# Kernel tuning notes

Measured on AMD Instinct MI355X. Metric: run time of the kernel, lower is better.

The kernel has to match this reference:

```python
import jax, jax.numpy as jnp
import numpy as np
import math

SENTINEL = 1.0e6  # eta/phi value assigned to inactive (pt<=0) objects
BIG = 1.0e6       # dR placeholder for non-lower-triangular entries


def _remove_duplicates(objs, threshold):
    """objs: (B, n, 3) with columns (pt, eta, phi). Zeros out objects that
    are within dR < threshold of a later object in the group (faithful to
    the TF strictly-lower-triangular / reduce over rows logic)."""
    n = objs.shape[1]
    active = objs[..., 0] > 0.0                              # (B, n)
    eta = jnp.where(active, objs[..., 1], SENTINEL)
    phi = jnp.where(active, objs[..., 2], SENTINEL)
    deta = eta[:, :, None] - eta[:, None, :]                 # (B, n, n)
    dphi = jnp.mod(phi[:, :, None] - phi[:, None, :] + math.pi,
                   2.0 * math.pi) - math.pi
    dr2 = deta * deta + dphi * dphi
    # strictly lower triangular mask (row i > col j), same as
    # logical_not(band_part(ones, 0, -1)) in TF
    tri = jnp.tril(jnp.ones((n, n), dtype=bool), k=-1)       # (n, n)
    # safe sqrt: only evaluate where the mask keeps the value
    dr = jnp.sqrt(jnp.where(tri, dr2, 1.0))
    replaced = jnp.where(tri, dr, BIG)                       # (B, n, n)
    # TF reduce_any(..., axis=0) per event -> axis=1 of batched tensor
    duplicates = jnp.any(replaced < threshold, axis=1)       # (B, n)
    return jnp.where(duplicates[..., None], 0.0, objs)


def duplicate_removal(x, threshold):
    jets = _remove_duplicates(x[:, 0:6], threshold)
    electrons = _remove_duplicates(x[:, 6:9], threshold)
    muons = _remove_duplicates(x[:, 9:12], threshold)
    photons = _remove_duplicates(x[:, 12:15], threshold)
    met = x[:, 15:16]
    return jnp.concatenate([jets, electrons, muons, photons, met], axis=1)


def setup_inputs() -> dict:
    key = jax.random.key(0)
    x = jax.random.normal(key, (1000000, 16, 3), dtype=jnp.float32)
    return {"x": x}


def reference(x):
    return duplicate_removal(x, 0.05)
```

## Files before the change

kernel.cpp:

```cpp
#include <hip/hip_runtime.h>
#include <math.h>

#define PI_F    3.14159274101257324e0f
#define TWOPI_F 6.28318548202514648e0f
#define SENT_F  1000000.0f

template <int OFF, int N>
__device__ __forceinline__ unsigned group_dup(const float* __restrict__ r) {
    float e[N], p[N];
#pragma unroll
    for (int k = 0; k < N; ++k) {
        float pt = r[3 * (OFF + k) + 0];
        bool act = pt > 0.0f;
        e[k] = act ? r[3 * (OFF + k) + 1] : SENT_F;
        p[k] = act ? r[3 * (OFF + k) + 2] : SENT_F;
    }
    unsigned dup = 0;
#pragma unroll
    for (int j = 0; j < N - 1; ++j) {
        bool d = false;
#pragma unroll
        for (int i = j + 1; i < N; ++i) {
            float deta = e[i] - e[j];
            float dd   = (p[i] - p[j]) + PI_F;
            float m    = fmodf(dd, TWOPI_F);
            m = (m < 0.0f) ? (m + TWOPI_F) : m;
            float dphi = m - PI_F;
            float dr2 = __fadd_rn(__fmul_rn(deta, deta), __fmul_rn(dphi, dphi));
            float dr  = __fsqrt_rn(dr2);
            d = d || (dr < 0.05f);
        }
        if (d) dup |= (1u << (OFF + j));
    }
    return dup;
}

__global__ __launch_bounds__(256) void dup_removal_kernel(
    const float4* __restrict__ in, float4* __restrict__ out, int B) {
    int row = blockIdx.x * blockDim.x + threadIdx.x;
    if (row >= B) return;

    const float4* src = in + (size_t)row * 12;
    float4* dst = out + (size_t)row * 12;

    float r[48];
#pragma unroll
    for (int k = 0; k < 12; ++k) {
        float4 v = src[k];
        r[4 * k + 0] = v.x;
        r[4 * k + 1] = v.y;
        r[4 * k + 2] = v.z;
        r[4 * k + 3] = v.w;
    }

    unsigned dup = 0;
    dup |= group_dup<0, 6>(r);
    dup |= group_dup<6, 3>(r);
    dup |= group_dup<9, 3>(r);
    dup |= group_dup<12, 3>(r);

#pragma unroll
    for (int o = 0; o < 15; ++o) {
        bool z = (dup >> o) & 1u;
        r[3 * o + 0] = z ? 0.0f : r[3 * o + 0];
        r[3 * o + 1] = z ? 0.0f : r[3 * o + 1];
        r[3 * o + 2] = z ? 0.0f : r[3 * o + 2];
    }

#pragma unroll
    for (int k = 0; k < 12; ++k) {
        float4 v;
        v.x = r[4 * k + 0];
        v.y = r[4 * k + 1];
        v.z = r[4 * k + 2];
        v.w = r[4 * k + 3];
        dst[k] = v;
    }
}

extern "C" void kernel_launch(void* const* d_in, const int* in_sizes, int n_in,
                              void* d_out, int out_size, void* d_ws, size_t ws_size,
                              hipStream_t stream) {
    const float4* x = (const float4*)d_in[0];
    float4* out = (float4*)d_out;
    int B = in_sizes[0] / 48;
    int block = 256;
    int grid = (B + block - 1) / block;
    dup_removal_kernel<<<grid, block, 0, stream>>>(x, out, B);
}
```

Before: 337.8 us.

## Stage rows through shared memory for coalesced global loads and stores

Each block loads its contiguous chunk of rows with thread-strided float4 reads into LDS, then each thread computes duplicates from its row in LDS. Per-row masks go to LDS, and output is written back in the same coalesced pattern with the mask applied per element. This replaces the per-thread 192-byte strided access that coalesced poorly. In exchange it uses 48 KB of LDS per block, limiting occupancy, and adds two barriers plus possible LDS bank conflicts on row reads.

```diff
diff --git a/kernel.cpp b/kernel.cpp
--- a/kernel.cpp
+++ b/kernel.cpp
@@ -6,7 +6,7 @@
 #define SENT_F  1000000.0f
 
 template <int OFF, int N>
-__device__ __forceinline__ unsigned group_dup(const float* __restrict__ r) {
+__device__ __forceinline__ unsigned group_dup(const float* r) {
     float e[N], p[N];
 #pragma unroll
     for (int k = 0; k < N; ++k) {
@@ -37,44 +37,52 @@
 
 __global__ __launch_bounds__(256) void dup_removal_kernel(
     const float4* __restrict__ in, float4* __restrict__ out, int B) {
-    int row = blockIdx.x * blockDim.x + threadIdx.x;
-    if (row >= B) return;
+    __shared__ float rowbuf[256 * 48];
+    __shared__ unsigned maskbuf[256];
 
-    const float4* src = in + (size_t)row * 12;
-    float4* dst = out + (size_t)row * 12;
+    const int t = threadIdx.x;
+    const long long base4  = (long long)blockIdx.x * 3072;
+    const long long total4 = (long long)B * 12;
 
-    float r[48];
+    float4 v[12];
 #pragma unroll
-    for (int k = 0; k < 12; ++k) {
-        float4 v = src[k];
-        r[4 * k + 0] = v.x;
-        r[4 * k + 1] = v.y;
-        r[4 * k + 2] = v.z;
-        r[4 * k + 3] = v.w;
+    for (int i = 0; i < 12; ++i) {
+        long long g = base4 + t + 256 * i;
+        if (g < total4) {
+            v[i] = in[g];
+            ((float4*)rowbuf)[t + 256 * i] = v[i];
+        }
     }
+    __syncthreads();
 
+    const int row = blockIdx.x * 256 + t;
     unsigned dup = 0;
-    dup |= group_dup<0, 6>(r);
-    dup |= group_dup<6, 3>(r);
-    dup |= group_dup<9, 3>(r);
-    dup |= group_dup<12, 3>(r);
+    if (row < B) {
+        const float* r = rowbuf + t * 48;
+        dup  = group_dup<0, 6>(r);
+        dup |= group_dup<6, 3>(r);
+        dup |= group_dup<9, 3>(r);
+        dup |= group_dup<12, 3>(r);
+    }
+    maskbuf[t] = dup;
+    __syncthreads();
 
 #pragma unroll
-    for (int o = 0; o < 15; ++o) {
-        bool z = (dup >> o) & 1u;
-        r[3 * o + 0] = z ? 0.0f : r[3 * o + 0];
-        r[3 * o + 1] = z ? 0.0f : r[3 * o + 1];
-        r[3 * o + 2] = z ? 0.0f : r[3 * o + 2];
-    }
-
-#pragma unroll
-    for (int k = 0; k < 12; ++k) {
-        float4 v;
-        v.x = r[4 * k + 0];
-        v.y = r[4 * k + 1];
-        v.z = r[4 * k + 2];
-        v.w = r[4 * k + 3];
-        dst[k] = v;
+    for (int i = 0; i < 12; ++i) {
+        long long g = base4 + t + 256 * i;
+        if (g < total4) {
+            int local = t + 256 * i;
+            int rl = local / 12;
+            int f  = local - rl * 12;
+            unsigned m = maskbuf[rl];
+            int k0 = 4 * f;
+            float4 w = v[i];
+            if ((m >> ((k0 + 0) / 3)) & 1u) w.x = 0.0f;
+            if ((m >> ((k0 + 1) / 3)) & 1u) w.y = 0.0f;
+            if ((m >> ((k0 + 2) / 3)) & 1u) w.z = 0.0f;
+            if ((m >> ((k0 + 3) / 3)) & 1u) w.w = 0.0f;
+            out[g] = w;
+        }
     }
 }
 
@@ -84,7 +92,6 @@
     const float4* x = (const float4*)d_in[0];
     float4* out = (float4*)d_out;
     int B = in_sizes[0] / 48;
-    int block = 256;
-    int grid = (B + block - 1) / block;
-    dup_removal_kernel<<<grid, block, 0, stream>>>(x, out, B);
+    int grid = (B + 255) / 256;
+    dup_removal_kernel<<<grid, 256, 0, stream>>>(x, out, B);
 }
```

New measurement: 349.2 us. 3.4% more time.
